# Kernel tuning notes

Measured on AMD Instinct MI355X. Metric: run time of the kernel, lower is better.

Reference implementation:

```python
import jax, jax.numpy as jnp
import numpy as np

D_MODEL = 128
NHEAD = 8
HEAD_DIM = D_MODEL // NHEAD  # 16
NUM_LAYERS = 7
NUM_LABELS = 2
N_NODES = 10000
N_EDGES = 160000
NEG_SLOPE = 0.2  # GATv2Conv default negative_slope


def setup_inputs() -> dict:
    key = jax.random.key(0)
    ks = jax.random.split(key, 10)
    s = 1.0 / np.sqrt(D_MODEL)
    inp = {}
    inp["x"] = jax.random.normal(ks[0], (N_NODES, D_MODEL), dtype=jnp.float32)
    inp["edge_index"] = jax.random.randint(ks[1], (2, N_EDGES), 0, N_NODES, dtype=jnp.int64)
    inp["nchunks"] = 8  # uniform extra chunk size -> chunk = NUM_LABELS + 8 = 10
    # per-layer GATv2 params, stacked on a leading layer axis
    inp["Wl"] = jax.random.normal(ks[2], (NUM_LAYERS, D_MODEL, NHEAD * HEAD_DIM), dtype=jnp.float32) * s
    inp["bl"] = jnp.zeros((NUM_LAYERS, NHEAD * HEAD_DIM), dtype=jnp.float32)
    inp["Wr"] = jax.random.normal(ks[3], (NUM_LAYERS, D_MODEL, NHEAD * HEAD_DIM), dtype=jnp.float32) * s
    inp["br"] = jnp.zeros((NUM_LAYERS, NHEAD * HEAD_DIM), dtype=jnp.float32)
    inp["att"] = jax.random.normal(ks[4], (NUM_LAYERS, NHEAD, HEAD_DIM), dtype=jnp.float32) * s
    inp["bias"] = jnp.zeros((NUM_LAYERS, NHEAD * HEAD_DIM), dtype=jnp.float32)
    # split head: Linear(d_model, 1)
    inp["w_head"] = jax.random.normal(ks[5], (D_MODEL, 1), dtype=jnp.float32) * s
    inp["b_head"] = jnp.zeros((1,), dtype=jnp.float32)
    return inp


def _gatv2_layer(x, src, dst, Wl, bl, Wr, br, att, bias):
    # GATv2: e_ij = a^T LeakyReLU(W_l x_j + W_r x_i); alpha = segment-softmax over dst; out_i = sum alpha * W_l x_j
    N = x.shape[0]
    xl = (x @ Wl + bl).reshape(N, NHEAD, HEAD_DIM)
    xr = (x @ Wr + br).reshape(N, NHEAD, HEAD_DIM)
    z = jax.nn.leaky_relu(xl[src] + xr[dst], NEG_SLOPE)          # [E, H, D]
    e = jnp.einsum('ehd,hd->eh', z, att)                          # [E, H]
    emax = jax.ops.segment_max(e, dst, num_segments=N)            # [N, H]
    ex = jnp.exp(e - emax[dst])
    denom = jax.ops.segment_sum(ex, dst, num_segments=N)          # [N, H]
    alpha = ex / (denom[dst] + 1e-16)                             # [E, H]
    out = jax.ops.segment_sum(alpha[..., None] * xl[src], dst, num_segments=N)  # [N, H, D]
    return out.reshape(N, NHEAD * HEAD_DIM) + bias


def reference(x, edge_index, nchunks, Wl, bl, Wr, br, att, bias, w_head, b_head):
    N = x.shape[0]
    loop = jnp.arange(N, dtype=edge_index.dtype)  # GATv2Conv add_self_loops=True
    src = jnp.concatenate([edge_index[0], loop])
    dst = jnp.concatenate([edge_index[1], loop])
    for i in range(NUM_LAYERS):
        x = _gatv2_layer(x, src, dst, Wl[i], bl[i], Wr[i], br[i], att[i], bias[i])
    # uniform split of size (NUM_LABELS + nchunks); keep first NUM_LABELS rows of each chunk
    chunk = NUM_LABELS + int(nchunks)
    xs = x.reshape(-1, chunk, D_MODEL)[:, :NUM_LABELS]            # [n_chunks, num_labels, d]
    out = (xs @ w_head + b_head)[..., 0]                          # [n_chunks, num_labels]
    return out
```

## Files before the change

kernel.cpp:

```cpp
#include <hip/hip_runtime.h>
#include <math.h>

#define NT 256

typedef __attribute__((ext_vector_type(8))) short bf16x8;
typedef __attribute__((ext_vector_type(4))) float f32x4;


__device__ inline int detect_is64(const int* __restrict__ ei) {
    int is64 = 1;
#pragma unroll
    for (int k = 1; k < 16; k += 2) is64 &= (ei[k] == 0);
    return is64;
}

__device__ inline void split1(float f, short& hi, short& lo) {
    unsigned u = __float_as_uint(f);
    hi = (short)(u >> 16);
    float fl = f - __uint_as_float(u & 0xffff0000u);
    lo = (short)(__float_as_uint(fl) >> 16);
}

__device__ inline void cvt8(const float4& a, const float4& b, bf16x8& hi, bf16x8& lo) {
    float f[8] = {a.x, a.y, a.z, a.w, b.x, b.y, b.z, b.w};
#pragma unroll
    for (int j = 0; j < 8; j++) {
        unsigned u = __float_as_uint(f[j]);
        hi[j] = (short)(u >> 16);
        float fl = f[j] - __uint_as_float(u & 0xffff0000u);
        lo[j] = (short)(__float_as_uint(fl) >> 16);
    }
}


__global__ void count_kernel(const int* __restrict__ ei, int E, int N, int* __restrict__ deg) {
    int e = blockIdx.x * blockDim.x + threadIdx.x;
    if (e >= E) return;
    int is64 = detect_is64(ei);
    long long pos = (long long)E + e;
    int d = ei[is64 ? 2 * pos : pos];
    if ((unsigned)d < (unsigned)N) atomicAdd(&deg[d], 1);
}

__global__ __launch_bounds__(256) void scan_kernel(const int* __restrict__ deg,
                                                   int* __restrict__ off,
                                                   int* __restrict__ cur, int N) {
    __shared__ int wsum[4];
    int t = threadIdx.x;
    int per = (N + 255) >> 8;
    int b0 = t * per;
    int s = 0;
    for (int k = 0; k < per; k++) {
        int idx = b0 + k;
        if (idx < N) s += deg[idx];
    }
    int lane = t & 63, w = t >> 6;
    int v = s;
#pragma unroll
    for (int o = 1; o < 64; o <<= 1) {
        int u = __shfl_up(v, o, 64);
        if (lane >= o) v += u;
    }
    if (lane == 63) wsum[w] = v;
    __syncthreads();
    if (t == 0) {
        int r = 0;
#pragma unroll
        for (int j = 0; j < 4; j++) { int xx = wsum[j]; wsum[j] = r; r += xx; }
        off[N] = r;
    }
    __syncthreads();
    int run = v - s + wsum[w];
    for (int k = 0; k < per; k++) {
        int idx = b0 + k;
        if (idx < N) {
            off[idx] = run;
            cur[idx] = run;
            run += deg[idx];
        }
    }
}

__global__ void fill_kernel(const int* __restrict__ ei, int E, int N,
                            int* __restrict__ cur, int* __restrict__ esrc) {
    int e = blockIdx.x * blockDim.x + threadIdx.x;
    if (e >= E) return;
    int is64 = detect_is64(ei);
    long long spos = e, dpos = (long long)E + e;
    int s = ei[is64 ? 2 * spos : spos];
    int d = ei[is64 ? 2 * dpos : dpos];
    if ((unsigned)d >= (unsigned)N || (unsigned)s >= (unsigned)N) return;
    int p = atomicAdd(&cur[d], 1);
    esrc[p] = s;
}


__global__ __launch_bounds__(256) void prep_w(const float* __restrict__ Wl,
                                              const float* __restrict__ Wr,
                                              short* __restrict__ Whi,
                                              short* __restrict__ Wlo) {
    __shared__ float Wt[128][17];
    int l = blockIdx.x >> 4;
    int tile = blockIdx.x & 15;
    int c0 = tile * 16;
    const float* Wsrc = (c0 < 128) ? Wl + (size_t)l * 16384 : Wr + (size_t)l * 16384;
    int cbase = (c0 < 128) ? c0 : c0 - 128;
    int t = threadIdx.x;
#pragma unroll
    for (int it = 0; it < 8; it++) {
        int idx = it * 256 + t;
        int k = idx >> 4, c = idx & 15;
        Wt[k][c] = Wsrc[(size_t)k * 128 + cbase + c];
    }
    __syncthreads();
    int kt = t >> 6, lane = t & 63, q = (lane >> 4), cl = lane & 15;
    bf16x8 hi, lo;
#pragma unroll
    for (int j = 0; j < 8; j++) {
        short h, lw;
        split1(Wt[kt * 32 + q * 8 + j][cl], h, lw);
        hi[j] = h; lo[j] = lw;
    }
    size_t off = ((((size_t)l * 16 + tile) * 4 + kt) * 64 + lane) * 8;
    *(bf16x8*)(Whi + off) = hi;
    *(bf16x8*)(Wlo + off) = lo;
}


__global__ __launch_bounds__(512, 1) void gemm_xlxr(const float* __restrict__ x,
                                                    const short* __restrict__ WhiL,
                                                    const short* __restrict__ WloL,
                                                    const float* __restrict__ blv,
                                                    const float* __restrict__ brv,
                                                    float* __restrict__ xl,
                                                    float* __restrict__ xr,
                                                    int N, int ntiles) {
    int t = threadIdx.x;
    int w = t >> 6, lane = t & 63, q = lane >> 4, cl = lane & 15;

    bf16x8 Bh[2][4], Bl[2][4];
    float biasv[2];
    float* outp[2];
    int colc[2];
#pragma unroll
    for (int nt = 0; nt < 2; nt++) {
        int tile = w * 2 + nt;
        int col = tile * 16 + cl;
        if (col < 128) { biasv[nt] = blv[col]; outp[nt] = xl; colc[nt] = col; }
        else           { biasv[nt] = brv[col - 128]; outp[nt] = xr; colc[nt] = col - 128; }
#pragma unroll
        for (int kt = 0; kt < 4; kt++) {
            size_t off = (((size_t)tile * 4 + kt) * 64 + lane) * 8;
            Bh[nt][kt] = *(const bf16x8*)(WhiL + off);
            Bl[nt][kt] = *(const bf16x8*)(WloL + off);
        }
    }

    int rt = blockIdx.x;
    if (rt >= ntiles) return;
    float4 cur[8], nxt[8];
    {
        int row = rt * 16 + cl;
        if (row >= N) row = N - 1;
        const float* ap = x + (size_t)row * 128 + q * 8;
#pragma unroll
        for (int kt = 0; kt < 4; kt++) {
            cur[2 * kt]     = *(const float4*)(ap + kt * 32);
            cur[2 * kt + 1] = *(const float4*)(ap + kt * 32 + 4);
        }
    }

    for (; rt < ntiles; rt += gridDim.x) {
        int rn = rt + gridDim.x;
        if (rn < ntiles) {
            int row = rn * 16 + cl;
            if (row >= N) row = N - 1;
            const float* ap = x + (size_t)row * 128 + q * 8;
#pragma unroll
            for (int kt = 0; kt < 4; kt++) {
                nxt[2 * kt]     = *(const float4*)(ap + kt * 32);
                nxt[2 * kt + 1] = *(const float4*)(ap + kt * 32 + 4);
            }
        }

        bf16x8 Ah[4], Al[4];
#pragma unroll
        for (int kt = 0; kt < 4; kt++) cvt8(cur[2 * kt], cur[2 * kt + 1], Ah[kt], Al[kt]);

        f32x4 acc0 = {0.f, 0.f, 0.f, 0.f}, acc1 = {0.f, 0.f, 0.f, 0.f};
#pragma unroll
        for (int kt = 0; kt < 4; kt++) {
            acc0 = __builtin_amdgcn_mfma_f32_16x16x32_bf16(Ah[kt], Bh[0][kt], acc0, 0, 0, 0);
            acc1 = __builtin_amdgcn_mfma_f32_16x16x32_bf16(Ah[kt], Bh[1][kt], acc1, 0, 0, 0);
            acc0 = __builtin_amdgcn_mfma_f32_16x16x32_bf16(Al[kt], Bh[0][kt], acc0, 0, 0, 0);
            acc1 = __builtin_amdgcn_mfma_f32_16x16x32_bf16(Al[kt], Bh[1][kt], acc1, 0, 0, 0);
            acc0 = __builtin_amdgcn_mfma_f32_16x16x32_bf16(Ah[kt], Bl[0][kt], acc0, 0, 0, 0);
            acc1 = __builtin_amdgcn_mfma_f32_16x16x32_bf16(Ah[kt], Bl[1][kt], acc1, 0, 0, 0);
        }

#pragma unroll
        for (int nt = 0; nt < 2; nt++) {
            f32x4 a = nt ? acc1 : acc0;
#pragma unroll
            for (int r = 0; r < 4; r++) {
                int row = rt * 16 + q * 4 + r;
                if (row < N) outp[nt][(size_t)row * 128 + colc[nt]] = a[r] + biasv[nt];
            }
        }
#pragma unroll
        for (int j = 0; j < 8; j++) cur[j] = nxt[j];
    }
}


__global__ __launch_bounds__(256) void gat_agg(const float4* __restrict__ xl4,
                                               const float4* __restrict__ xr4,
                                               const int* __restrict__ off,
                                               const int* __restrict__ esrc,
                                               const float4* __restrict__ att4,
                                               const float4* __restrict__ bias4,
                                               float4* __restrict__ out4, int N) {
    int lane = threadIdx.x & 63;
    int sub = lane >> 4;
    int cl = lane & 15;
    int i = blockIdx.x * 4 + (threadIdx.x >> 6);
    if (i >= N) return;

    float4 xrA = xr4[(size_t)i * 32 + 2 * cl];
    float4 xrB = xr4[(size_t)i * 32 + 2 * cl + 1];
    float4 atA = att4[2 * cl];
    float4 atB = att4[2 * cl + 1];
    int start = off[i];
    int total = off[i + 1] - start + 1;
    int groups = (total + 3) >> 2;

    int k0 = sub;
    int s0 = (k0 < total) ? ((k0 == 0) ? i : esrc[start + k0 - 1]) : i;
    int k1 = 4 + sub;
    int s1 = (k1 < total) ? esrc[start + k1 - 1] : i;
    float4 v0A = xl4[(size_t)s0 * 32 + 2 * cl];
    float4 v0B = xl4[(size_t)s0 * 32 + 2 * cl + 1];
    int k2 = 8 + sub;
    int s2 = (k2 < total) ? esrc[start + k2 - 1] : i;
    float4 v1A = xl4[(size_t)s1 * 32 + 2 * cl];
    float4 v1B = xl4[(size_t)s1 * 32 + 2 * cl + 1];

    float s = 0.f;
    float4 aA = make_float4(0.f, 0.f, 0.f, 0.f);
    float4 aB = make_float4(0.f, 0.f, 0.f, 0.f);

    for (int g = 0; g < groups; g++) {
        int k3 = 4 * (g + 3) + sub;
        int s3 = (k3 < total) ? esrc[start + k3 - 1] : i;
        float4 v2A = xl4[(size_t)s2 * 32 + 2 * cl];
        float4 v2B = xl4[(size_t)s2 * 32 + 2 * cl + 1];

        int kc = 4 * g + sub;
        int valid = kc < total;
        float z0 = v0A.x + xrA.x, z1 = v0A.y + xrA.y, z2 = v0A.z + xrA.z, z3 = v0A.w + xrA.w;
        float z4 = v0B.x + xrB.x, z5 = v0B.y + xrB.y, z6 = v0B.z + xrB.z, z7 = v0B.w + xrB.w;
        z0 = (z0 > 0.f) ? z0 : 0.2f * z0;
        z1 = (z1 > 0.f) ? z1 : 0.2f * z1;
        z2 = (z2 > 0.f) ? z2 : 0.2f * z2;
        z3 = (z3 > 0.f) ? z3 : 0.2f * z3;
        z4 = (z4 > 0.f) ? z4 : 0.2f * z4;
        z5 = (z5 > 0.f) ? z5 : 0.2f * z5;
        z6 = (z6 > 0.f) ? z6 : 0.2f * z6;
        z7 = (z7 > 0.f) ? z7 : 0.2f * z7;
        float p = z0 * atA.x + z1 * atA.y + z2 * atA.z + z3 * atA.w
                + z4 * atB.x + z5 * atB.y + z6 * atB.z + z7 * atB.w;
        p += __shfl_xor(p, 1, 64);
        p = fminf(fmaxf(p, -80.f), 80.f);
        float wgt = valid ? __expf(p) : 0.f;
        s += wgt;
        aA.x += wgt * v0A.x; aA.y += wgt * v0A.y; aA.z += wgt * v0A.z; aA.w += wgt * v0A.w;
        aB.x += wgt * v0B.x; aB.y += wgt * v0B.y; aB.z += wgt * v0B.z; aB.w += wgt * v0B.w;

        v0A = v1A; v0B = v1B;
        v1A = v2A; v1B = v2B;
        s2 = s3;
    }

#pragma unroll
    for (int o = 16; o <= 32; o <<= 1) {
        s += __shfl_xor(s, o, 64);
        aA.x += __shfl_xor(aA.x, o, 64); aA.y += __shfl_xor(aA.y, o, 64);
        aA.z += __shfl_xor(aA.z, o, 64); aA.w += __shfl_xor(aA.w, o, 64);
        aB.x += __shfl_xor(aB.x, o, 64); aB.y += __shfl_xor(aB.y, o, 64);
        aB.z += __shfl_xor(aB.z, o, 64); aB.w += __shfl_xor(aB.w, o, 64);
    }
    if (sub == 0) {
        float inv = 1.f / (s + 1e-16f);
        float4 bA = bias4[2 * cl], bB = bias4[2 * cl + 1];
        float4 oA, oB;
        oA.x = aA.x * inv + bA.x; oA.y = aA.y * inv + bA.y;
        oA.z = aA.z * inv + bA.z; oA.w = aA.w * inv + bA.w;
        oB.x = aB.x * inv + bB.x; oB.y = aB.y * inv + bB.y;
        oB.z = aB.z * inv + bB.z; oB.w = aB.w * inv + bB.w;
        out4[(size_t)i * 32 + 2 * cl] = oA;
        out4[(size_t)i * 32 + 2 * cl + 1] = oB;
    }
}


__global__ __launch_bounds__(128) void head_kernel(const float* __restrict__ x,
                                                   const float* __restrict__ w,
                                                   const float* __restrict__ bh,
                                                   const int* __restrict__ nch,
                                                   float* __restrict__ out) {
    __shared__ float r[2];
    int b = blockIdx.x, t = threadIdx.x;
    int chunk = 2 + nch[0];
    int row = (b >> 1) * chunk + (b & 1);
    float p = x[(size_t)row * 128 + t] * w[t];
#pragma unroll
    for (int o = 32; o >= 1; o >>= 1) p += __shfl_xor(p, o, 64);
    if ((t & 63) == 0) r[t >> 6] = p;
    __syncthreads();
    if (t == 0) out[b] = r[0] + r[1] + bh[0];
}


extern "C" void kernel_launch(void* const* d_in, const int* in_sizes, int n_in,
                              void* d_out, int out_size, void* d_ws, size_t ws_size,
                              hipStream_t stream) {
    const float* x0 = (const float*)d_in[0];
    const int* ei = (const int*)d_in[1];
    const int* nchunks = (const int*)d_in[2];
    const float* Wl = (const float*)d_in[3];
    const float* bl = (const float*)d_in[4];
    const float* Wr = (const float*)d_in[5];
    const float* br = (const float*)d_in[6];
    const float* att = (const float*)d_in[7];
    const float* bias = (const float*)d_in[8];
    const float* wh = (const float*)d_in[9];
    const float* bh = (const float*)d_in[10];

    const int D = 128;
    int N = in_sizes[0] / D;
    int E = in_sizes[1] / 2;
    int ntiles = (N + 15) / 16;

    size_t fN = (size_t)N * D;
    const size_t WFRAG = 16 * 4 * 64 * 8;
    float* xl = (float*)d_ws;
    float* xr = xl + fN;
    float* xA = xr + fN;
    float* xB = xA + fN;
    short* Whi = (short*)(xB + fN);
    short* Wlo = Whi + 7 * WFRAG;
    int* deg = (int*)(Wlo + 7 * WFRAG);
    int* off = deg + N;
    int* cur = off + N + 1;
    int* esrc = cur + N;

    hipMemsetAsync(deg, 0, (size_t)N * sizeof(int), stream);
    prep_w<<<112, 256, 0, stream>>>(Wl, Wr, Whi, Wlo);
    count_kernel<<<(E + NT - 1) / NT, NT, 0, stream>>>(ei, E, N, deg);
    scan_kernel<<<1, 256, 0, stream>>>(deg, off, cur, N);
    fill_kernel<<<(E + NT - 1) / NT, NT, 0, stream>>>(ei, E, N, cur, esrc);

    int aggblocks = (N + 3) / 4;
    const float* xc = x0;
    float* xn = xA;
    for (int l = 0; l < 7; l++) {
        gemm_xlxr<<<256, 512, 0, stream>>>(xc, Whi + (size_t)l * WFRAG, Wlo + (size_t)l * WFRAG,
                                           bl + (size_t)l * D, br + (size_t)l * D,
                                           xl, xr, N, ntiles);
        gat_agg<<<aggblocks, 256, 0, stream>>>((const float4*)xl, (const float4*)xr, off, esrc,
                                               (const float4*)(att + (size_t)l * D),
                                               (const float4*)(bias + (size_t)l * D),
                                               (float4*)xn, N);
        xc = xn;
        xn = (xn == xA) ? xB : xA;
    }
    head_kernel<<<out_size, 128, 0, stream>>>(xc, wh, bh, nchunks, (float*)d_out);
}
```

Before: 315.0 us.

## Fuse per-layer aggregation with next layer's projection GEMM and merge prologue kernels

Each layer's attention aggregation now feeds the next layer's Wl/Wr projection inside one kernel. The aggregated 16-node tile is converted to split bf16 in shared memory and multiplied with MFMA, so the intermediate x is never written to or read back from global memory. The weight prep, input conversion and degree counting are merged into a single prologue kernel, and the scan uses 1024 threads. This cuts kernel launches and global traffic. The cost is that each fused block reloads the weight fragments from global memory and runs the GEMM with low per-block parallelism after a barrier that waits on uneven per-node aggregation work.

```diff
diff --git a/kernel.cpp b/kernel.cpp
--- a/kernel.cpp
+++ b/kernel.cpp
@@ -1,10 +1,10 @@
 #include <hip/hip_runtime.h>
 #include <math.h>
 
-#define NT 256
-
 typedef __attribute__((ext_vector_type(8))) short bf16x8;
 typedef __attribute__((ext_vector_type(4))) float f32x4;
+
+#define WFRAG (16 * 4 * 64 * 8)
 
 
 __device__ inline int detect_is64(const int* __restrict__ ei) {
@@ -33,21 +33,70 @@
 }
 
 
-__global__ void count_kernel(const int* __restrict__ ei, int E, int N, int* __restrict__ deg) {
-    int e = blockIdx.x * blockDim.x + threadIdx.x;
-    if (e >= E) return;
+__global__ __launch_bounds__(256) void prologue(const float* __restrict__ Wl,
+                                                const float* __restrict__ Wr,
+                                                short* __restrict__ Whi,
+                                                short* __restrict__ Wlo,
+                                                const float4* __restrict__ x4,
+                                                short* __restrict__ cvH,
+                                                short* __restrict__ cvL,
+                                                const int* __restrict__ ei,
+                                                int* __restrict__ deg,
+                                                int N, int E) {
+    __shared__ float Wt[128][17];
+    int b = blockIdx.x, t = threadIdx.x;
+    if (b < 112) {
+        int l = b >> 4;
+        int tile = b & 15;
+        int c0 = tile * 16;
+        const float* Wsrc = (c0 < 128) ? Wl + (size_t)l * 16384 : Wr + (size_t)l * 16384;
+        int cbase = (c0 < 128) ? c0 : c0 - 128;
+#pragma unroll
+        for (int it = 0; it < 8; it++) {
+            int idx = it * 256 + t;
+            int k = idx >> 4, c = idx & 15;
+            Wt[k][c] = Wsrc[(size_t)k * 128 + cbase + c];
+        }
+        __syncthreads();
+        int kt = t >> 6, lane = t & 63, q = (lane >> 4), cl = lane & 15;
+        bf16x8 hi, lo;
+#pragma unroll
+        for (int j = 0; j < 8; j++) {
+            short h, lw;
+            split1(Wt[kt * 32 + q * 8 + j][cl], h, lw);
+            hi[j] = h; lo[j] = lw;
+        }
+        size_t off = ((((size_t)l * 16 + tile) * 4 + kt) * 64 + lane) * 8;
+        *(bf16x8*)(Whi + off) = hi;
+        *(bf16x8*)(Wlo + off) = lo;
+        return;
+    }
+    int rb = b - 112;
+    int RB = gridDim.x - 112;
+    int n8 = N * 16;
+    for (int id = rb * 256 + t; id < n8; id += RB * 256) {
+        float4 a = x4[2 * id];
+        float4 bb = x4[2 * id + 1];
+        bf16x8 h, lw;
+        cvt8(a, bb, h, lw);
+        *(bf16x8*)(cvH + (size_t)id * 8) = h;
+        *(bf16x8*)(cvL + (size_t)id * 8) = lw;
+    }
     int is64 = detect_is64(ei);
-    long long pos = (long long)E + e;
-    int d = ei[is64 ? 2 * pos : pos];
-    if ((unsigned)d < (unsigned)N) atomicAdd(&deg[d], 1);
-}
-
-__global__ __launch_bounds__(256) void scan_kernel(const int* __restrict__ deg,
-                                                   int* __restrict__ off,
-                                                   int* __restrict__ cur, int N) {
-    __shared__ int wsum[4];
+    for (int e = rb * 256 + t; e < E; e += RB * 256) {
+        long long pos = (long long)E + e;
+        int d = ei[is64 ? 2 * pos : pos];
+        if ((unsigned)d < (unsigned)N) atomicAdd(&deg[d], 1);
+    }
+}
+
+
+__global__ __launch_bounds__(1024) void scan_kernel(const int* __restrict__ deg,
+                                                    int* __restrict__ off,
+                                                    int* __restrict__ cur, int N) {
+    __shared__ int wsum[16];
     int t = threadIdx.x;
-    int per = (N + 255) >> 8;
+    int per = (N + 1023) >> 10;
     int b0 = t * per;
     int s = 0;
     for (int k = 0; k < per; k++) {
@@ -66,7 +115,7 @@
     if (t == 0) {
         int r = 0;
 #pragma unroll
-        for (int j = 0; j < 4; j++) { int xx = wsum[j]; wsum[j] = r; r += xx; }
+        for (int j = 0; j < 16; j++) { int xx = wsum[j]; wsum[j] = r; r += xx; }
         off[N] = r;
     }
     __syncthreads();
@@ -95,39 +144,8 @@
 }
 
 
-__global__ __launch_bounds__(256) void prep_w(const float* __restrict__ Wl,
-                                              const float* __restrict__ Wr,
-                                              short* __restrict__ Whi,
-                                              short* __restrict__ Wlo) {
-    __shared__ float Wt[128][17];
-    int l = blockIdx.x >> 4;
-    int tile = blockIdx.x & 15;
-    int c0 = tile * 16;
-    const float* Wsrc = (c0 < 128) ? Wl + (size_t)l * 16384 : Wr + (size_t)l * 16384;
-    int cbase = (c0 < 128) ? c0 : c0 - 128;
-    int t = threadIdx.x;
-#pragma unroll
-    for (int it = 0; it < 8; it++) {
-        int idx = it * 256 + t;
-        int k = idx >> 4, c = idx & 15;
-        Wt[k][c] = Wsrc[(size_t)k * 128 + cbase + c];
-    }
-    __syncthreads();
-    int kt = t >> 6, lane = t & 63, q = (lane >> 4), cl = lane & 15;
-    bf16x8 hi, lo;
-#pragma unroll
-    for (int j = 0; j < 8; j++) {
-        short h, lw;
-        split1(Wt[kt * 32 + q * 8 + j][cl], h, lw);
-        hi[j] = h; lo[j] = lw;
-    }
-    size_t off = ((((size_t)l * 16 + tile) * 4 + kt) * 64 + lane) * 8;
-    *(bf16x8*)(Whi + off) = hi;
-    *(bf16x8*)(Wlo + off) = lo;
-}
-
-
-__global__ __launch_bounds__(512, 1) void gemm_xlxr(const float* __restrict__ x,
+__global__ __launch_bounds__(512, 1) void gemm_xlxr(const short* __restrict__ xhi,
+                                                    const short* __restrict__ xlo,
                                                     const short* __restrict__ WhiL,
                                                     const short* __restrict__ WloL,
                                                     const float* __restrict__ blv,
@@ -140,62 +158,43 @@
 
     bf16x8 Bh[2][4], Bl[2][4];
     float biasv[2];
-    float* outp[2];
+    float* op[2];
     int colc[2];
 #pragma unroll
     for (int nt = 0; nt < 2; nt++) {
         int tile = w * 2 + nt;
         int col = tile * 16 + cl;
-        if (col < 128) { biasv[nt] = blv[col]; outp[nt] = xl; colc[nt] = col; }
-        else           { biasv[nt] = brv[col - 128]; outp[nt] = xr; colc[nt] = col - 128; }
+        if (col < 128) { biasv[nt] = blv[col]; op[nt] = xl; colc[nt] = col; }
+        else           { biasv[nt] = brv[col - 128]; op[nt] = xr; colc[nt] = col - 128; }
 #pragma unroll
         for (int kt = 0; kt < 4; kt++) {
-            size_t off = (((size_t)tile * 4 + kt) * 64 + lane) * 8;
-            Bh[nt][kt] = *(const bf16x8*)(WhiL + off);
-            Bl[nt][kt] = *(const bf16x8*)(WloL + off);
-        }
-    }
-
-    int rt = blockIdx.x;
-    if (rt >= ntiles) return;
-    float4 cur[8], nxt[8];
-    {
+            size_t o = (((size_t)tile * 4 + kt) * 64 + lane) * 8;
+            Bh[nt][kt] = *(const bf16x8*)(WhiL + o);
+            Bl[nt][kt] = *(const bf16x8*)(WloL + o);
+        }
+    }
+
+    for (int rt = blockIdx.x; rt < ntiles; rt += gridDim.x) {
         int row = rt * 16 + cl;
         if (row >= N) row = N - 1;
-        const float* ap = x + (size_t)row * 128 + q * 8;
+        const short* ph = xhi + (size_t)row * 128 + q * 8;
+        const short* pl = xlo + (size_t)row * 128 + q * 8;
+        bf16x8 AH[4], AL[4];
 #pragma unroll
         for (int kt = 0; kt < 4; kt++) {
-            cur[2 * kt]     = *(const float4*)(ap + kt * 32);
-            cur[2 * kt + 1] = *(const float4*)(ap + kt * 32 + 4);
-        }
-    }
-
-    for (; rt < ntiles; rt += gridDim.x) {
-        int rn = rt + gridDim.x;
-        if (rn < ntiles) {
-            int row = rn * 16 + cl;
-            if (row >= N) row = N - 1;
-            const float* ap = x + (size_t)row * 128 + q * 8;
-#pragma unroll
-            for (int kt = 0; kt < 4; kt++) {
-                nxt[2 * kt]     = *(const float4*)(ap + kt * 32);
-                nxt[2 * kt + 1] = *(const float4*)(ap + kt * 32 + 4);
-            }
-        }
-
-        bf16x8 Ah[4], Al[4];
-#pragma unroll
-        for (int kt = 0; kt < 4; kt++) cvt8(cur[2 * kt], cur[2 * kt + 1], Ah[kt], Al[kt]);
+            AH[kt] = *(const bf16x8*)(ph + kt * 32);
+            AL[kt] = *(const bf16x8*)(pl + kt * 32);
+        }
 
         f32x4 acc0 = {0.f, 0.f, 0.f, 0.f}, acc1 = {0.f, 0.f, 0.f, 0.f};
 #pragma unroll
         for (int kt = 0; kt < 4; kt++) {
-            acc0 = __builtin_amdgcn_mfma_f32_16x16x32_bf16(Ah[kt], Bh[0][kt], acc0, 0, 0, 0);
-            acc1 = __builtin_amdgcn_mfma_f32_16x16x32_bf16(Ah[kt], Bh[1][kt], acc1, 0, 0, 0);
-            acc0 = __builtin_amdgcn_mfma_f32_16x16x32_bf16(Al[kt], Bh[0][kt], acc0, 0, 0, 0);
-            acc1 = __builtin_amdgcn_mfma_f32_16x16x32_bf16(Al[kt], Bh[1][kt], acc1, 0, 0, 0);
-            acc0 = __builtin_amdgcn_mfma_f32_16x16x32_bf16(Ah[kt], Bl[0][kt], acc0, 0, 0, 0);
-            acc1 = __builtin_amdgcn_mfma_f32_16x16x32_bf16(Ah[kt], Bl[1][kt], acc1, 0, 0, 0);
+            acc0 = __builtin_amdgcn_mfma_f32_16x16x32_bf16(AH[kt], Bh[0][kt], acc0, 0, 0, 0);
+            acc1 = __builtin_amdgcn_mfma_f32_16x16x32_bf16(AH[kt], Bh[1][kt], acc1, 0, 0, 0);
+            acc0 = __builtin_amdgcn_mfma_f32_16x16x32_bf16(AL[kt], Bh[0][kt], acc0, 0, 0, 0);
+            acc1 = __builtin_amdgcn_mfma_f32_16x16x32_bf16(AL[kt], Bh[1][kt], acc1, 0, 0, 0);
+            acc0 = __builtin_amdgcn_mfma_f32_16x16x32_bf16(AH[kt], Bl[0][kt], acc0, 0, 0, 0);
+            acc1 = __builtin_amdgcn_mfma_f32_16x16x32_bf16(AH[kt], Bl[1][kt], acc1, 0, 0, 0);
         }
 
 #pragma unroll
@@ -203,33 +202,21 @@
             f32x4 a = nt ? acc1 : acc0;
 #pragma unroll
             for (int r = 0; r < 4; r++) {
-                int row = rt * 16 + q * 4 + r;
-                if (row < N) outp[nt][(size_t)row * 128 + colc[nt]] = a[r] + biasv[nt];
+                int orow = rt * 16 + q * 4 + r;
+                if (orow < N) op[nt][(size_t)orow * 128 + colc[nt]] = a[r] + biasv[nt];
             }
         }
-#pragma unroll
-        for (int j = 0; j < 8; j++) cur[j] = nxt[j];
-    }
-}
-
-
-__global__ __launch_bounds__(256) void gat_agg(const float4* __restrict__ xl4,
-                                               const float4* __restrict__ xr4,
-                                               const int* __restrict__ off,
-                                               const int* __restrict__ esrc,
-                                               const float4* __restrict__ att4,
-                                               const float4* __restrict__ bias4,
-                                               float4* __restrict__ out4, int N) {
-    int lane = threadIdx.x & 63;
-    int sub = lane >> 4;
-    int cl = lane & 15;
-    int i = blockIdx.x * 4 + (threadIdx.x >> 6);
-    if (i >= N) return;
-
+    }
+}
+
+
+__device__ inline void agg_node(int i, int sub, int cl,
+                                const float4* __restrict__ xl4, const float4* __restrict__ xr4,
+                                const int* __restrict__ off, const int* __restrict__ esrc,
+                                float4 atA, float4 atB, float4 bA, float4 bB,
+                                float4& oA, float4& oB) {
     float4 xrA = xr4[(size_t)i * 32 + 2 * cl];
     float4 xrB = xr4[(size_t)i * 32 + 2 * cl + 1];
-    float4 atA = att4[2 * cl];
-    float4 atB = att4[2 * cl + 1];
     int start = off[i];
     int total = off[i + 1] - start + 1;
     int groups = (total + 3) >> 2;
@@ -289,14 +276,106 @@
         aB.x += __shfl_xor(aB.x, o, 64); aB.y += __shfl_xor(aB.y, o, 64);
         aB.z += __shfl_xor(aB.z, o, 64); aB.w += __shfl_xor(aB.w, o, 64);
     }
+    float inv = 1.f / (s + 1e-16f);
+    oA.x = aA.x * inv + bA.x; oA.y = aA.y * inv + bA.y;
+    oA.z = aA.z * inv + bA.z; oA.w = aA.w * inv + bA.w;
+    oB.x = aB.x * inv + bB.x; oB.y = aB.y * inv + bB.y;
+    oB.z = aB.z * inv + bB.z; oB.w = aB.w * inv + bB.w;
+}
+
+
+__global__ __launch_bounds__(256) void agg_gemm(const float4* __restrict__ xl4,
+                                                const float4* __restrict__ xr4,
+                                                const int* __restrict__ off,
+                                                const int* __restrict__ esrc,
+                                                const float4* __restrict__ att4,
+                                                const float4* __restrict__ bias4,
+                                                const short* __restrict__ WhiL,
+                                                const short* __restrict__ WloL,
+                                                const float* __restrict__ blv,
+                                                const float* __restrict__ brv,
+                                                float* __restrict__ xlo_out,
+                                                float* __restrict__ xro_out,
+                                                int N) {
+    __shared__ __align__(16) short hiL[16 * 136];
+    __shared__ __align__(16) short loL[16 * 136];
+    int t = threadIdx.x;
+    int w = t >> 6, lane = t & 63, sub = lane >> 4, cl = lane & 15, q = lane >> 4;
+    int base = blockIdx.x * 16;
+
+    float4 atA = att4[2 * cl];
+    float4 atB = att4[2 * cl + 1];
+    float4 bA = bias4[2 * cl], bB = bias4[2 * cl + 1];
+
+    for (int j = 0; j < 4; j++) {
+        int i = base + w * 4 + j;
+        if (i < N) {
+            float4 oA, oB;
+            agg_node(i, sub, cl, xl4, xr4, off, esrc, atA, atB, bA, bB, oA, oB);
+            if (sub == 0) {
+                bf16x8 h, lw;
+                cvt8(oA, oB, h, lw);
+                int r = w * 4 + j;
+                *(bf16x8*)&hiL[r * 136 + cl * 8] = h;
+                *(bf16x8*)&loL[r * 136 + cl * 8] = lw;
+            }
+        }
+    }
+    __syncthreads();
+
+    bf16x8 Ah[4], Al[4];
+#pragma unroll
+    for (int kt = 0; kt < 4; kt++) {
+        Ah[kt] = *(const bf16x8*)&hiL[cl * 136 + kt * 32 + q * 8];
+        Al[kt] = *(const bf16x8*)&loL[cl * 136 + kt * 32 + q * 8];
+    }
+
+#pragma unroll
+    for (int tt = 0; tt < 4; tt++) {
+        int tile = w * 4 + tt;
+        int col = tile * 16 + cl;
+        f32x4 acc = {0.f, 0.f, 0.f, 0.f};
+#pragma unroll
+        for (int kt = 0; kt < 4; kt++) {
+            size_t o = (((size_t)tile * 4 + kt) * 64 + lane) * 8;
+            bf16x8 bh = *(const bf16x8*)(WhiL + o);
+            bf16x8 bl2 = *(const bf16x8*)(WloL + o);
+            acc = __builtin_amdgcn_mfma_f32_16x16x32_bf16(Ah[kt], bh, acc, 0, 0, 0);
+            acc = __builtin_amdgcn_mfma_f32_16x16x32_bf16(Al[kt], bh, acc, 0, 0, 0);
+            acc = __builtin_amdgcn_mfma_f32_16x16x32_bf16(Ah[kt], bl2, acc, 0, 0, 0);
+        }
+        float biasv;
+        float* op;
+        int cc;
+        if (col < 128) { biasv = blv[col]; op = xlo_out; cc = col; }
+        else           { biasv = brv[col - 128]; op = xro_out; cc = col - 128; }
+#pragma unroll
+        for (int r = 0; r < 4; r++) {
+            int row = base + q * 4 + r;
+            if (row < N) op[(size_t)row * 128 + cc] = acc[r] + biasv;
+        }
+    }
+}
+
+
+__global__ __launch_bounds__(256) void gat_agg(const float4* __restrict__ xl4,
+                                               const float4* __restrict__ xr4,
+                                               const int* __restrict__ off,
+                                               const int* __restrict__ esrc,
+                                               const float4* __restrict__ att4,
+                                               const float4* __restrict__ bias4,
+                                               float4* __restrict__ out4, int N) {
+    int lane = threadIdx.x & 63;
+    int sub = lane >> 4;
+    int cl = lane & 15;
+    int i = blockIdx.x * 4 + (threadIdx.x >> 6);
+    if (i >= N) return;
+    float4 atA = att4[2 * cl];
+    float4 atB = att4[2 * cl + 1];
+    float4 bA = bias4[2 * cl], bB = bias4[2 * cl + 1];
+    float4 oA, oB;
+    agg_node(i, sub, cl, xl4, xr4, off, esrc, atA, atB, bA, bB, oA, oB);
     if (sub == 0) {
-        float inv = 1.f / (s + 1e-16f);
-        float4 bA = bias4[2 * cl], bB = bias4[2 * cl + 1];
-        float4 oA, oB;
-        oA.x = aA.x * inv + bA.x; oA.y = aA.y * inv + bA.y;
-        oA.z = aA.z * inv + bA.z; oA.w = aA.w * inv + bA.w;
-        oB.x = aB.x * inv + bB.x; oB.y = aB.y * inv + bB.y;
-        oB.z = aB.z * inv + bB.z; oB.w = aB.w * inv + bB.w;
         out4[(size_t)i * 32 + 2 * cl] = oA;
         out4[(size_t)i * 32 + 2 * cl + 1] = oB;
     }
@@ -342,37 +421,47 @@
     int ntiles = (N + 15) / 16;
 
     size_t fN = (size_t)N * D;
-    const size_t WFRAG = 16 * 4 * 64 * 8;
-    float* xl = (float*)d_ws;
-    float* xr = xl + fN;
-    float* xA = xr + fN;
-    float* xB = xA + fN;
-    short* Whi = (short*)(xB + fN);
-    short* Wlo = Whi + 7 * WFRAG;
-    int* deg = (int*)(Wlo + 7 * WFRAG);
+    float* xlA = (float*)d_ws;
+    float* xrA = xlA + fN;
+    float* xlB = xrA + fN;
+    float* xrB = xlB + fN;
+    float* xout = xrB + fN;
+    short* cvH0 = (short*)(xout + fN);
+    short* cvL0 = cvH0 + fN;
+    short* Whi = cvL0 + fN;
+    short* Wlo = Whi + 7 * (size_t)WFRAG;
+    int* deg = (int*)(Wlo + 7 * (size_t)WFRAG);
     int* off = deg + N;
     int* cur = off + N + 1;
     int* esrc = cur + N;
 
     hipMemsetAsync(deg, 0, (size_t)N * sizeof(int), stream);
-    prep_w<<<112, 256, 0, stream>>>(Wl, Wr, Whi, Wlo);
-    count_kernel<<<(E + NT - 1) / NT, NT, 0, stream>>>(ei, E, N, deg);
-    scan_kernel<<<1, 256, 0, stream>>>(deg, off, cur, N);
-    fill_kernel<<<(E + NT - 1) / NT, NT, 0, stream>>>(ei, E, N, cur, esrc);
-
-    int aggblocks = (N + 3) / 4;
-    const float* xc = x0;
-    float* xn = xA;
-    for (int l = 0; l < 7; l++) {
-        gemm_xlxr<<<256, 512, 0, stream>>>(xc, Whi + (size_t)l * WFRAG, Wlo + (size_t)l * WFRAG,
-                                           bl + (size_t)l * D, br + (size_t)l * D,
-                                           xl, xr, N, ntiles);
-        gat_agg<<<aggblocks, 256, 0, stream>>>((const float4*)xl, (const float4*)xr, off, esrc,
-                                               (const float4*)(att + (size_t)l * D),
-                                               (const float4*)(bias + (size_t)l * D),
-                                               (float4*)xn, N);
-        xc = xn;
-        xn = (xn == xA) ? xB : xA;
-    }
-    head_kernel<<<out_size, 128, 0, stream>>>(xc, wh, bh, nchunks, (float*)d_out);
-}
+    prologue<<<112 + 640, 256, 0, stream>>>(Wl, Wr, Whi, Wlo, (const float4*)x0,
+                                            cvH0, cvL0, ei, deg, N, E);
+    scan_kernel<<<1, 1024, 0, stream>>>(deg, off, cur, N);
+    fill_kernel<<<(E + 255) / 256, 256, 0, stream>>>(ei, E, N, cur, esrc);
+
+    gemm_xlxr<<<256, 512, 0, stream>>>(cvH0, cvL0, Whi, Wlo, bl, br, xlA, xrA, N, ntiles);
+
+    for (int l = 0; l < 6; l++) {
+        const float* rxl = (l % 2 == 0) ? xlA : xlB;
+        const float* rxr = (l % 2 == 0) ? xrA : xrB;
+        float* wxl = (l % 2 == 0) ? xlB : xlA;
+        float* wxr = (l % 2 == 0) ? xrB : xrA;
+        agg_gemm<<<ntiles, 256, 0, stream>>>((const float4*)rxl, (const float4*)rxr, off, esrc,
+                                             (const float4*)(att + (size_t)l * D),
+                                             (const float4*)(bias + (size_t)l * D),
+                                             Whi + (size_t)(l + 1) * WFRAG,
+                                             Wlo + (size_t)(l + 1) * WFRAG,
+                                             bl + (size_t)(l + 1) * D,
+                                             br + (size_t)(l + 1) * D,
+                                             wxl, wxr, N);
+    }
+
+    gat_agg<<<(N + 3) / 4, 256, 0, stream>>>((const float4*)xlA, (const float4*)xrA, off, esrc,
+                                             (const float4*)(att + 6 * (size_t)D),
+                                             (const float4*)(bias + 6 * (size_t)D),
+                                             (float4*)xout, N);
+
+    head_kernel<<<out_size, 128, 0, stream>>>(xout, wh, bh, nchunks, (float*)d_out);
+}
```

Result: faster. 272.8 us (-13.4%).
